# Kernel optimization log

Measured on AMD Instinct MI355X. Metric: run time of the kernel, lower is better.

Reference implementation:

```python
import jax, jax.numpy as jnp
import numpy as np

N = 100000      # nodes
E = 1000000     # edges per relation
D_IN = 128
D_OUT = 128
SLOPE = 0.2
N_REL = 3


def setup_inputs() -> dict:
    key = jax.random.key(0)
    ks = jax.random.split(key, 1 + 4 * N_REL)
    inp = {"H": jax.random.normal(ks[0], (N, D_IN), dtype=jnp.float32)}
    xav_w = float(np.sqrt(6.0 / (D_IN + D_OUT)))   # xavier_uniform bound for W
    xav_a = float(np.sqrt(6.0 / (1 + 2 * D_OUT)))  # xavier_uniform on a viewed as [1, 2d]
    for i in range(N_REL):
        inp[f"row_{i}"] = jax.random.randint(ks[1 + 4 * i], (E,), 0, N, dtype=jnp.int64)
        inp[f"col_{i}"] = jax.random.randint(ks[2 + 4 * i], (E,), 0, N, dtype=jnp.int64)
        inp[f"W_{i}"] = jax.random.uniform(ks[3 + 4 * i], (D_IN, D_OUT), jnp.float32, -xav_w, xav_w)
        inp[f"a_{i}"] = jax.random.uniform(ks[4 + 4 * i], (2 * D_OUT,), jnp.float32, -xav_a, xav_a)
    inp["bias"] = jnp.zeros((D_OUT,), jnp.float32)
    return inp


def _relation_agg(H, W, a, row, col):
    # 1) transform: Wh = H @ W_r  [N, d]
    Wh = H @ W
    d = Wh.shape[1]
    # 2) edge scores: e_ij = leaky_relu(a[:d].Wh[row] + a[d:].Wh[col])
    s_dst = Wh @ a[:d]   # coefficient for destination (row) side  [N]
    s_src = Wh @ a[d:]   # coefficient for source (col) side       [N]
    e = jax.nn.leaky_relu(s_dst[row] + s_src[col], negative_slope=SLOPE)  # [E]
    # 3) segment softmax over incoming edges of each destination node
    e_max = jax.ops.segment_max(e, row, num_segments=N)          # [N]
    e_shift = jnp.exp(e - e_max[row])                            # [E]
    e_sum = jax.ops.segment_sum(e_shift, row, num_segments=N)    # [N]
    alpha = e_shift / jnp.maximum(e_sum[row], 1e-12)             # [E]
    # 4) weighted aggregation of source features
    return jax.ops.segment_sum(alpha[:, None] * Wh[col], row, num_segments=N)  # [N, d]


def reference(H, row_0, col_0, row_1, col_1, row_2, col_2,
              W_0, W_1, W_2, a_0, a_1, a_2, bias):
    rows = (row_0, row_1, row_2)
    cols = (col_0, col_1, col_2)
    Ws = (W_0, W_1, W_2)
    As = (a_0, a_1, a_2)
    agg = jnp.zeros((N, D_OUT), H.dtype)
    for r in range(N_REL):
        agg = agg + _relation_agg(H, Ws[r], As[r], rows[r], cols[r])
    return agg + bias
```

## Files before the change

kernel.cpp:

```cpp
#include <hip/hip_runtime.h>

#define SLOPE 0.2f

typedef unsigned int uint;
typedef unsigned short ushort;
typedef __attribute__((ext_vector_type(8))) short short8;
typedef __attribute__((ext_vector_type(4))) float f32x4;

#define BINW 2048
#define BINSHIFT 11
#define CAP 22528

__device__ inline ushort f2bf(float f) {
    uint u = __float_as_uint(f);
    uint r = (u + 0x7FFFu + ((u >> 16) & 1u)) >> 16;
    return (ushort)r;
}
__device__ inline uint pack2bf(float lo, float hi) {
    return (uint)f2bf(lo) | ((uint)f2bf(hi) << 16);
}
__device__ inline float bfl(uint u) { return __uint_as_float(u << 16); }
__device__ inline float bfh(uint u) { return __uint_as_float(u & 0xFFFF0000u); }

__global__ void wt3(const float* __restrict__ W0, const float* __restrict__ W1,
                    const float* __restrict__ W2,
                    const float* __restrict__ a0, const float* __restrict__ a1,
                    const float* __restrict__ a2,
                    ushort* __restrict__ WT, float* __restrict__ wa,
                    int* __restrict__ bincnt, int nbz) {
    int r = blockIdx.x;
    if (r == 0 && threadIdx.x < nbz) bincnt[threadIdx.x] = 0;
    const float* W = (r == 0) ? W0 : (r == 1) ? W1 : W2;
    const float* a = (r == 0) ? a0 : (r == 1) ? a1 : a2;
    ushort* wt = WT + r * 16384;
    for (int i = threadIdx.x; i < 16384; i += 256) {
        int k = i >> 7, n = i & 127;
        wt[n * 128 + k] = f2bf(W[i]);
    }
    if (threadIdx.x < 128) {
        int k = threadIdx.x;
        const float* wrow = W + k * 128;
        float pd = 0.f, ps = 0.f;
        for (int n = 0; n < 128; n += 4) {
            float4 w4 = *reinterpret_cast<const float4*>(wrow + n);
            float4 aL = *reinterpret_cast<const float4*>(a + n);
            float4 aR = *reinterpret_cast<const float4*>(a + 128 + n);
            pd += w4.x * aL.x + w4.y * aL.y + w4.z * aL.z + w4.w * aL.w;
            ps += w4.x * aR.x + w4.y * aR.y + w4.z * aR.z + w4.w * aR.w;
        }
        wa[r * 256 + k] = pd;
        wa[r * 256 + 128 + k] = ps;
    }
}

__global__ __launch_bounds__(256) void gemm3(const float* __restrict__ H,
                                             const ushort* __restrict__ WT,
                                             ushort* __restrict__ whAll, int N) {
    __shared__ ushort lds[16384];
    const int brow = blockIdx.x * 128;
    const int t = threadIdx.x;

    for (int c = t; c < 2048; c += 256) {
        int r = c >> 4;
        int kb = (c & 15) << 4;
        int gr = brow + r;
        uint4 u = make_uint4(0, 0, 0, 0);
        if (gr < N) {
            const float* hp = H + (size_t)gr * 128 + (kb >> 1);
            float4 v0 = *reinterpret_cast<const float4*>(hp);
            float4 v1 = *reinterpret_cast<const float4*>(hp + 4);
            u.x = pack2bf(v0.x, v0.y);
            u.y = pack2bf(v0.z, v0.w);
            u.z = pack2bf(v1.x, v1.y);
            u.w = pack2bf(v1.z, v1.w);
        }
        int dst = (r << 8) + (kb ^ ((r & 7) << 4));
        *reinterpret_cast<uint4*>((char*)lds + dst) = u;
    }
    __syncthreads();

    const int wave = t >> 6, lane = t & 63;
    const int l16 = lane & 15, lhi = lane >> 4;

    for (int rel = 0; rel < 3; ++rel) {
        ushort* Wh = whAll + (size_t)rel * N * 128;
        const ushort* wt = WT + rel * 16384;

        short8 bf[2][4];
#pragma unroll
        for (int nt = 0; nt < 2; ++nt) {
            int n = wave * 32 + nt * 16 + l16;
#pragma unroll
            for (int ks = 0; ks < 4; ++ks)
                bf[nt][ks] = *reinterpret_cast<const short8*>(wt + n * 128 + ks * 32 + lhi * 8);
        }

        f32x4 acc[8][2];
#pragma unroll
        for (int mt = 0; mt < 8; ++mt) { acc[mt][0] = (f32x4)(0.f); acc[mt][1] = (f32x4)(0.f); }

#pragma unroll
        for (int ks = 0; ks < 4; ++ks) {
#pragma unroll
            for (int mt = 0; mt < 8; ++mt) {
                int r = mt * 16 + l16;
                int kb = (ks * 32 + lhi * 8) * 2;
                int addr = (r << 8) + (kb ^ ((r & 7) << 4));
                short8 af = *reinterpret_cast<const short8*>((char*)lds + addr);
                acc[mt][0] = __builtin_amdgcn_mfma_f32_16x16x32_bf16(af, bf[0][ks], acc[mt][0], 0, 0, 0);
                acc[mt][1] = __builtin_amdgcn_mfma_f32_16x16x32_bf16(af, bf[1][ks], acc[mt][1], 0, 0, 0);
            }
        }

#pragma unroll
        for (int mt = 0; mt < 8; ++mt)
#pragma unroll
            for (int nt = 0; nt < 2; ++nt)
#pragma unroll
                for (int reg = 0; reg < 4; ++reg) {
                    int gr = brow + mt * 16 + lhi * 4 + reg;
                    if (gr < N)
                        Wh[(size_t)gr * 128 + wave * 32 + nt * 16 + l16] = f2bf(acc[mt][nt][reg]);
                }
    }
}

__global__ __launch_bounds__(256) void scores_k(const float* __restrict__ H,
                                                const float* __restrict__ wa,
                                                float* __restrict__ sd,
                                                float* __restrict__ ss, int N) {
    int node = blockIdx.x * 16 + (threadIdx.x >> 4);
    int ql = threadIdx.x & 15;
    if (node >= N) return;
    const float* hp = H + (size_t)node * 128 + ql * 8;
    float4 h0 = *reinterpret_cast<const float4*>(hp);
    float4 h1 = *reinterpret_cast<const float4*>(hp + 4);
#pragma unroll
    for (int r = 0; r < 3; ++r) {
        const float* wd = wa + r * 256 + ql * 8;
        const float* wsv = wa + r * 256 + 128 + ql * 8;
        float4 d0 = *reinterpret_cast<const float4*>(wd);
        float4 d1 = *reinterpret_cast<const float4*>(wd + 4);
        float4 s0 = *reinterpret_cast<const float4*>(wsv);
        float4 s1 = *reinterpret_cast<const float4*>(wsv + 4);
        float pd = h0.x * d0.x + h0.y * d0.y + h0.z * d0.z + h0.w * d0.w +
                   h1.x * d1.x + h1.y * d1.y + h1.z * d1.z + h1.w * d1.w;
        float ps = h0.x * s0.x + h0.y * s0.y + h0.z * s0.z + h0.w * s0.w +
                   h1.x * s1.x + h1.y * s1.y + h1.z * s1.z + h1.w * s1.w;
#pragma unroll
        for (int off = 1; off < 16; off <<= 1) {
            pd += __shfl_xor(pd, off);
            ps += __shfl_xor(ps, off);
        }
        if (ql == 0) { sd[r * N + node] = pd; ss[r * N + node] = ps; }
    }
}

__global__ __launch_bounds__(256) void binscatter(const int* __restrict__ r0, const int* __restrict__ r1,
                                                  const int* __restrict__ r2, const int* __restrict__ c0,
                                                  const int* __restrict__ c1, const int* __restrict__ c2,
                                                  const float* __restrict__ sd, const float* __restrict__ ss,
                                                  int* __restrict__ bincnt, uint2* __restrict__ binned,
                                                  int E, int N, int nbins) {
    __shared__ uint2 staged[4096];
    __shared__ int hist[256], sB[256], curi[256], gbase[256];
    const int t = threadIdx.x;
    hist[t] = 0;
    __syncthreads();

    uint2 rec[16];
    short bn[16];
    const int base = blockIdx.x * 4096;
#pragma unroll
    for (int k = 0; k < 16; ++k) {
        int i = base + k * 256 + t;
        bn[k] = -1;
        if (i < 3 * E) {
            int r = (i >= 2 * E) ? 2 : (i >= E) ? 1 : 0;
            int li = i - r * E;
            const int* rp = (r == 0) ? r0 : (r == 1) ? r1 : r2;
            const int* cp = (r == 0) ? c0 : (r == 1) ? c1 : c2;
            int rr = __builtin_nontemporal_load(rp + li);
            int cc = __builtin_nontemporal_load(cp + li);
            int idx = rr * 3 + r;
            int b = idx >> BINSHIFT;
            uint lo = (uint)(idx & (BINW - 1));
            float x = sd[r * N + rr] + ss[r * N + cc];
            x = (x > 0.f) ? x : SLOPE * x;
            float w = __expf(x);
            rec[k] = make_uint2((uint)cc | (lo << 17), __float_as_uint(w));
            bn[k] = (short)b;
            atomicAdd(&hist[b], 1);
        }
    }
    __syncthreads();

    int v = hist[t];
    int* pa = hist; int* pb = sB;
    for (int off = 1; off < 256; off <<= 1) {
        int x = pa[t] + ((t >= off) ? pa[t - off] : 0);
        pb[t] = x;
        __syncthreads();
        int* tmp = pa; pa = pb; pb = tmp;
    }
    sB[t] = pa[t] - v;
    curi[t] = pa[t] - v;
    if (t < nbins && v > 0) gbase[t] = t * CAP + atomicAdd(&bincnt[t], v);
    __syncthreads();

#pragma unroll
    for (int k = 0; k < 16; ++k)
        if (bn[k] >= 0) {
            int p = atomicAdd(&curi[bn[k]], 1);
            staged[p] = rec[k];
        }
    __syncthreads();

    const int g32 = t >> 5, lane32 = t & 31;
    for (int b = g32; b < nbins; b += 8) {
        int s = sB[b];
        int len = hist[b] - s;
        if (len <= 0) continue;
        int g = gbase[b];
        for (int j = lane32; j < len; j += 32) binned[g + j] = staged[s + j];
    }
}

__global__ __launch_bounds__(256) void binscan(const int* __restrict__ bincnt,
                                               int* __restrict__ binbase, int nbins) {
    __shared__ int sA[256], sB[256];
    int t = threadIdx.x;
    int v = (t < nbins) ? bincnt[t] : 0;
    sA[t] = v;
    __syncthreads();
    int* pa = sA; int* pb = sB;
    for (int off = 1; off < 256; off <<= 1) {
        int x = pa[t] + ((t >= off) ? pa[t - off] : 0);
        pb[t] = x;
        __syncthreads();
        int* tmp = pa; pa = pb; pb = tmp;
    }
    if (t < nbins) binbase[t] = pa[t] - v;
    if (t == nbins - 1) binbase[nbins] = pa[t];
}

__global__ __launch_bounds__(256) void binsort(const uint2* __restrict__ binned,
                                               const int* __restrict__ bincnt,
                                               const int* __restrict__ binbase,
                                               uint2* __restrict__ wc, int* __restrict__ offs,
                                               int L, int N) {
    __shared__ int s1[BINW];
    __shared__ int wsum[4];
    const int b = blockIdx.x, t = threadIdx.x;
    const int cnt = bincnt[b];
    const int dst0 = binbase[b];
    const uint2* src = binned + (size_t)b * CAP;
    const int ibase = b << BINSHIFT;
    const int width = min(BINW, L - ibase);

    for (int i = t; i < BINW; i += 256) s1[i] = 0;
    __syncthreads();
    for (int j = t; j < cnt; j += 256)
        atomicAdd(&s1[(src[j].x >> 17) & (BINW - 1)], 1);
    __syncthreads();

    const int cb = t * 8;
    int v[8];
    int run = 0;
#pragma unroll
    for (int k = 0; k < 8; ++k) { run += s1[cb + k]; v[k] = run; }
    const int lane = t & 63, wv = t >> 6;
    int x = run;
#pragma unroll
    for (int off = 1; off < 64; off <<= 1) {
        int y = __shfl_up(x, off);
        if (lane >= off) x += y;
    }
    if (lane == 63) wsum[wv] = x;
    __syncthreads();
    int pre = x - run;
#pragma unroll
    for (int w = 0; w < 3; ++w) if (wv > w) pre += wsum[w];

#pragma unroll
    for (int k = 0; k < 8; ++k) {
        int i = cb + k;
        if (i < width) offs[ibase + i] = dst0 + pre + v[k];
    }
#pragma unroll
    for (int k = 0; k < 8; ++k)
        s1[cb + k] = dst0 + pre + (k ? v[k - 1] : 0);
    __syncthreads();

    for (int j = t; j < cnt; j += 256) {
        uint2 r = src[j];
        uint lo = (r.x >> 17) & (BINW - 1);
        int p = atomicAdd(&s1[lo], 1);
        int gidx = ibase + (int)lo;
        int rel = gidx - (gidx / 3) * 3;
        uint cc = r.x & 0x1FFFFu;
        wc[p] = make_uint2(r.y, ((uint)(rel * N) + cc) | ((uint)rel << 19));
    }
}

__global__ __launch_bounds__(256) void aggregate3(const uint* __restrict__ whAll,
                                                  const uint2* __restrict__ wc,
                                                  const int* __restrict__ offs,
                                                  const float* __restrict__ bias,
                                                  float* __restrict__ out, int N) {
    int node = blockIdx.x * 16 + (threadIdx.x >> 4);
    int ql = threadIdx.x & 15;
    if (node >= N) return;

    const int base = node * 3;
    const int s0 = (base == 0) ? 0 : offs[base - 1];
    const int s3 = offs[base + 2];

    float w0s = 0.f, w1s = 0.f, w2s = 0.f;
    for (int j = s0; j < s3; ++j) {
        uint2 e = wc[j];
        float w = __uint_as_float(e.x);
        uint rel = e.y >> 19;
        w0s += (rel == 0) ? w : 0.f;
        w1s += (rel == 1) ? w : 0.f;
        w2s += (rel == 2) ? w : 0.f;
    }
    const float inv0 = 1.f / fmaxf(w0s, 1e-12f);
    const float inv1 = 1.f / fmaxf(w1s, 1e-12f);
    const float inv2 = 1.f / fmaxf(w2s, 1e-12f);

    float a0 = 0.f, a1 = 0.f, a2 = 0.f, a3 = 0.f, a4 = 0.f, a5 = 0.f, a6 = 0.f, a7 = 0.f;
    float g0 = 0.f, g1 = 0.f, g2 = 0.f, g3 = 0.f, g4 = 0.f, g5 = 0.f, g6 = 0.f, g7 = 0.f;

    int j = s0;
    for (; j + 4 <= s3; j += 4) {
        uint2 e0 = wc[j], e1 = wc[j + 1], e2 = wc[j + 2], e3 = wc[j + 3];
        uint4 v0 = reinterpret_cast<const uint4*>(whAll + ((size_t)(e0.y & 0x7FFFFu) << 6))[ql];
        uint4 v1 = reinterpret_cast<const uint4*>(whAll + ((size_t)(e1.y & 0x7FFFFu) << 6))[ql];
        uint4 v2 = reinterpret_cast<const uint4*>(whAll + ((size_t)(e2.y & 0x7FFFFu) << 6))[ql];
        uint4 v3 = reinterpret_cast<const uint4*>(whAll + ((size_t)(e3.y & 0x7FFFFu) << 6))[ql];
        uint r0 = e0.y >> 19, r1 = e1.y >> 19, r2 = e2.y >> 19, r3 = e3.y >> 19;
        float w0 = __uint_as_float(e0.x) * ((r0 == 0) ? inv0 : (r0 == 1) ? inv1 : inv2);
        float w1 = __uint_as_float(e1.x) * ((r1 == 0) ? inv0 : (r1 == 1) ? inv1 : inv2);
        float w2 = __uint_as_float(e2.x) * ((r2 == 0) ? inv0 : (r2 == 1) ? inv1 : inv2);
        float w3 = __uint_as_float(e3.x) * ((r3 == 0) ? inv0 : (r3 == 1) ? inv1 : inv2);
        a0 = fmaf(w0, bfl(v0.x), a0); a1 = fmaf(w0, bfh(v0.x), a1);
        a2 = fmaf(w0, bfl(v0.y), a2); a3 = fmaf(w0, bfh(v0.y), a3);
        a4 = fmaf(w0, bfl(v0.z), a4); a5 = fmaf(w0, bfh(v0.z), a5);
        a6 = fmaf(w0, bfl(v0.w), a6); a7 = fmaf(w0, bfh(v0.w), a7);
        g0 = fmaf(w1, bfl(v1.x), g0); g1 = fmaf(w1, bfh(v1.x), g1);
        g2 = fmaf(w1, bfl(v1.y), g2); g3 = fmaf(w1, bfh(v1.y), g3);
        g4 = fmaf(w1, bfl(v1.z), g4); g5 = fmaf(w1, bfh(v1.z), g5);
        g6 = fmaf(w1, bfl(v1.w), g6); g7 = fmaf(w1, bfh(v1.w), g7);
        a0 = fmaf(w2, bfl(v2.x), a0); a1 = fmaf(w2, bfh(v2.x), a1);
        a2 = fmaf(w2, bfl(v2.y), a2); a3 = fmaf(w2, bfh(v2.y), a3);
        a4 = fmaf(w2, bfl(v2.z), a4); a5 = fmaf(w2, bfh(v2.z), a5);
        a6 = fmaf(w2, bfl(v2.w), a6); a7 = fmaf(w2, bfh(v2.w), a7);
        g0 = fmaf(w3, bfl(v3.x), g0); g1 = fmaf(w3, bfh(v3.x), g1);
        g2 = fmaf(w3, bfl(v3.y), g2); g3 = fmaf(w3, bfh(v3.y), g3);
        g4 = fmaf(w3, bfl(v3.z), g4); g5 = fmaf(w3, bfh(v3.z), g5);
        g6 = fmaf(w3, bfl(v3.w), g6); g7 = fmaf(w3, bfh(v3.w), g7);
    }
    for (; j < s3; ++j) {
        uint2 e = wc[j];
        uint r = e.y >> 19;
        float w = __uint_as_float(e.x) * ((r == 0) ? inv0 : (r == 1) ? inv1 : inv2);
        uint4 v = reinterpret_cast<const uint4*>(whAll + ((size_t)(e.y & 0x7FFFFu) << 6))[ql];
        a0 = fmaf(w, bfl(v.x), a0); a1 = fmaf(w, bfh(v.x), a1);
        a2 = fmaf(w, bfl(v.y), a2); a3 = fmaf(w, bfh(v.y), a3);
        a4 = fmaf(w, bfl(v.z), a4); a5 = fmaf(w, bfh(v.z), a5);
        a6 = fmaf(w, bfl(v.w), a6); a7 = fmaf(w, bfh(v.w), a7);
    }

    float4 b0 = *reinterpret_cast<const float4*>(bias + ql * 8);
    float4 b1 = *reinterpret_cast<const float4*>(bias + ql * 8 + 4);
    float* o = out + (size_t)node * 128 + ql * 8;
    f32x4 o0 = {a0 + g0 + b0.x, a1 + g1 + b0.y, a2 + g2 + b0.z, a3 + g3 + b0.w};
    f32x4 o1 = {a4 + g4 + b1.x, a5 + g5 + b1.y, a6 + g6 + b1.z, a7 + g7 + b1.w};
    __builtin_nontemporal_store(o0, reinterpret_cast<f32x4*>(o));
    __builtin_nontemporal_store(o1, reinterpret_cast<f32x4*>(o + 4));
}

extern "C" void kernel_launch(void* const* d_in, const int* in_sizes, int n_in,
                              void* d_out, int out_size, void* d_ws, size_t ws_size,
                              hipStream_t stream) {
    const float* H = (const float*)d_in[0];
    const int* row[3] = {(const int*)d_in[1], (const int*)d_in[5], (const int*)d_in[9]};
    const int* col[3] = {(const int*)d_in[2], (const int*)d_in[6], (const int*)d_in[10]};
    const float* W[3] = {(const float*)d_in[3], (const float*)d_in[7], (const float*)d_in[11]};
    const float* a[3] = {(const float*)d_in[4], (const float*)d_in[8], (const float*)d_in[12]};
    const float* bias = (const float*)d_in[13];

    const int N = in_sizes[0] / 128;
    const int E = in_sizes[1];
    float* out = (float*)d_out;

    const int L = 3 * N;
    const int nbins = (L + BINW - 1) >> BINSHIFT;

    char* ws = (char*)d_ws;
    size_t off = 0;
    auto alloc = [&](size_t bytes) -> void* {
        void* p = ws + off;
        off += (bytes + 255) & ~(size_t)255;
        return p;
    };

    ushort* WT = (ushort*)alloc(3 * 16384 * 2);
    float* wa = (float*)alloc(3 * 256 * 4);
    ushort* whAll = (ushort*)alloc((size_t)3 * N * 128 * 2);
    float* sd = (float*)alloc((size_t)L * 4);
    float* ss = (float*)alloc((size_t)L * 4);
    int* offs = (int*)alloc((size_t)L * 4);
    int* bincnt = (int*)alloc((size_t)(nbins + 2) * 4);
    int* binbase = (int*)alloc((size_t)(nbins + 2) * 4);
    uint2* wc = (uint2*)alloc((size_t)3 * E * 8);
    uint2* binned = (uint2*)d_out;

    const int nbG = (N + 127) / 128;
    const int nbQ = (N + 15) / 16;
    const int nbB = (3 * E + 4095) / 4096;

    wt3<<<3, 256, 0, stream>>>(W[0], W[1], W[2], a[0], a[1], a[2], WT, wa, bincnt, nbins + 2);
    gemm3<<<nbG, 256, 0, stream>>>(H, WT, whAll, N);
    scores_k<<<nbQ, 256, 0, stream>>>(H, wa, sd, ss, N);

    binscatter<<<nbB, 256, 0, stream>>>(row[0], row[1], row[2], col[0], col[1], col[2],
                                        sd, ss, bincnt, binned, E, N, nbins);
    binscan<<<1, 256, 0, stream>>>(bincnt, binbase, nbins);
    binsort<<<nbins, 256, 0, stream>>>(binned, bincnt, binbase, wc, offs, L, N);

    aggregate3<<<nbQ, 256, 0, stream>>>((const uint*)whAll, wc, offs, bias, out, N);
}
```

Measured before the change: 330.8 us.

## Bin edges by relation-major key and fuse softmax normalization into aggregation

Changes the CSR bucketing key from node*3+rel to rel*N+node, so each (relation, destination) segment is contiguous and the relation can be recovered from the bucket range instead of stored bits. The aggregation kernel now walks each relation's segment once, accumulating the softmax denominator alongside the weighted feature sum, and applies the normalization afterwards. This removes the separate first pass over edges that only computed per-relation weight sums. A node's three relation segments are no longer adjacent in memory, and the per-node work now goes through a three-iteration loop with separate bounds loads.

```diff
diff --git a/kernel.cpp b/kernel.cpp
--- a/kernel.cpp
+++ b/kernel.cpp
@@ -182,10 +182,10 @@
             const int* cp = (r == 0) ? c0 : (r == 1) ? c1 : c2;
             int rr = __builtin_nontemporal_load(rp + li);
             int cc = __builtin_nontemporal_load(cp + li);
-            int idx = rr * 3 + r;
+            int idx = r * N + rr;
             int b = idx >> BINSHIFT;
             uint lo = (uint)(idx & (BINW - 1));
-            float x = sd[r * N + rr] + ss[r * N + cc];
+            float x = sd[idx] + ss[r * N + cc];
             x = (x > 0.f) ? x : SLOPE * x;
             float w = __expf(x);
             rec[k] = make_uint2((uint)cc | (lo << 17), __float_as_uint(w));
@@ -297,9 +297,9 @@
         uint lo = (r.x >> 17) & (BINW - 1);
         int p = atomicAdd(&s1[lo], 1);
         int gidx = ibase + (int)lo;
-        int rel = gidx - (gidx / 3) * 3;
+        int rel = (gidx >= 2 * N) ? 2 : (gidx >= N) ? 1 : 0;
         uint cc = r.x & 0x1FFFFu;
-        wc[p] = make_uint2(r.y, ((uint)(rel * N) + cc) | ((uint)rel << 19));
+        wc[p] = make_uint2(r.y, (uint)(rel * N) + cc);
     }
 }
 
@@ -312,71 +312,69 @@
     int ql = threadIdx.x & 15;
     if (node >= N) return;
 
-    const int base = node * 3;
-    const int s0 = (base == 0) ? 0 : offs[base - 1];
-    const int s3 = offs[base + 2];
-
-    float w0s = 0.f, w1s = 0.f, w2s = 0.f;
-    for (int j = s0; j < s3; ++j) {
-        uint2 e = wc[j];
-        float w = __uint_as_float(e.x);
-        uint rel = e.y >> 19;
-        w0s += (rel == 0) ? w : 0.f;
-        w1s += (rel == 1) ? w : 0.f;
-        w2s += (rel == 2) ? w : 0.f;
-    }
-    const float inv0 = 1.f / fmaxf(w0s, 1e-12f);
-    const float inv1 = 1.f / fmaxf(w1s, 1e-12f);
-    const float inv2 = 1.f / fmaxf(w2s, 1e-12f);
-
-    float a0 = 0.f, a1 = 0.f, a2 = 0.f, a3 = 0.f, a4 = 0.f, a5 = 0.f, a6 = 0.f, a7 = 0.f;
-    float g0 = 0.f, g1 = 0.f, g2 = 0.f, g3 = 0.f, g4 = 0.f, g5 = 0.f, g6 = 0.f, g7 = 0.f;
-
-    int j = s0;
-    for (; j + 4 <= s3; j += 4) {
-        uint2 e0 = wc[j], e1 = wc[j + 1], e2 = wc[j + 2], e3 = wc[j + 3];
-        uint4 v0 = reinterpret_cast<const uint4*>(whAll + ((size_t)(e0.y & 0x7FFFFu) << 6))[ql];
-        uint4 v1 = reinterpret_cast<const uint4*>(whAll + ((size_t)(e1.y & 0x7FFFFu) << 6))[ql];
-        uint4 v2 = reinterpret_cast<const uint4*>(whAll + ((size_t)(e2.y & 0x7FFFFu) << 6))[ql];
-        uint4 v3 = reinterpret_cast<const uint4*>(whAll + ((size_t)(e3.y & 0x7FFFFu) << 6))[ql];
-        uint r0 = e0.y >> 19, r1 = e1.y >> 19, r2 = e2.y >> 19, r3 = e3.y >> 19;
-        float w0 = __uint_as_float(e0.x) * ((r0 == 0) ? inv0 : (r0 == 1) ? inv1 : inv2);
-        float w1 = __uint_as_float(e1.x) * ((r1 == 0) ? inv0 : (r1 == 1) ? inv1 : inv2);
-        float w2 = __uint_as_float(e2.x) * ((r2 == 0) ? inv0 : (r2 == 1) ? inv1 : inv2);
-        float w3 = __uint_as_float(e3.x) * ((r3 == 0) ? inv0 : (r3 == 1) ? inv1 : inv2);
-        a0 = fmaf(w0, bfl(v0.x), a0); a1 = fmaf(w0, bfh(v0.x), a1);
-        a2 = fmaf(w0, bfl(v0.y), a2); a3 = fmaf(w0, bfh(v0.y), a3);
-        a4 = fmaf(w0, bfl(v0.z), a4); a5 = fmaf(w0, bfh(v0.z), a5);
-        a6 = fmaf(w0, bfl(v0.w), a6); a7 = fmaf(w0, bfh(v0.w), a7);
-        g0 = fmaf(w1, bfl(v1.x), g0); g1 = fmaf(w1, bfh(v1.x), g1);
-        g2 = fmaf(w1, bfl(v1.y), g2); g3 = fmaf(w1, bfh(v1.y), g3);
-        g4 = fmaf(w1, bfl(v1.z), g4); g5 = fmaf(w1, bfh(v1.z), g5);
-        g6 = fmaf(w1, bfl(v1.w), g6); g7 = fmaf(w1, bfh(v1.w), g7);
-        a0 = fmaf(w2, bfl(v2.x), a0); a1 = fmaf(w2, bfh(v2.x), a1);
-        a2 = fmaf(w2, bfl(v2.y), a2); a3 = fmaf(w2, bfh(v2.y), a3);
-        a4 = fmaf(w2, bfl(v2.z), a4); a5 = fmaf(w2, bfh(v2.z), a5);
-        a6 = fmaf(w2, bfl(v2.w), a6); a7 = fmaf(w2, bfh(v2.w), a7);
-        g0 = fmaf(w3, bfl(v3.x), g0); g1 = fmaf(w3, bfh(v3.x), g1);
-        g2 = fmaf(w3, bfl(v3.y), g2); g3 = fmaf(w3, bfh(v3.y), g3);
-        g4 = fmaf(w3, bfl(v3.z), g4); g5 = fmaf(w3, bfh(v3.z), g5);
-        g6 = fmaf(w3, bfl(v3.w), g6); g7 = fmaf(w3, bfh(v3.w), g7);
-    }
-    for (; j < s3; ++j) {
-        uint2 e = wc[j];
-        uint r = e.y >> 19;
-        float w = __uint_as_float(e.x) * ((r == 0) ? inv0 : (r == 1) ? inv1 : inv2);
-        uint4 v = reinterpret_cast<const uint4*>(whAll + ((size_t)(e.y & 0x7FFFFu) << 6))[ql];
-        a0 = fmaf(w, bfl(v.x), a0); a1 = fmaf(w, bfh(v.x), a1);
-        a2 = fmaf(w, bfl(v.y), a2); a3 = fmaf(w, bfh(v.y), a3);
-        a4 = fmaf(w, bfl(v.z), a4); a5 = fmaf(w, bfh(v.z), a5);
-        a6 = fmaf(w, bfl(v.w), a6); a7 = fmaf(w, bfh(v.w), a7);
+    float t0 = 0.f, t1 = 0.f, t2 = 0.f, t3 = 0.f, t4 = 0.f, t5 = 0.f, t6 = 0.f, t7 = 0.f;
+
+#pragma unroll
+    for (int r = 0; r < 3; ++r) {
+        int idx = r * N + node;
+        int end = offs[idx];
+        int beg = (idx == 0) ? 0 : offs[idx - 1];
+        if (beg >= end) continue;
+
+        float wsA = 0.f, wsB = 0.f;
+        float a0 = 0.f, a1 = 0.f, a2 = 0.f, a3 = 0.f, a4 = 0.f, a5 = 0.f, a6 = 0.f, a7 = 0.f;
+        float g0 = 0.f, g1 = 0.f, g2 = 0.f, g3 = 0.f, g4 = 0.f, g5 = 0.f, g6 = 0.f, g7 = 0.f;
+
+        int j = beg;
+        for (; j + 4 <= end; j += 4) {
+            uint2 e0 = wc[j], e1 = wc[j + 1], e2 = wc[j + 2], e3 = wc[j + 3];
+            uint4 v0 = reinterpret_cast<const uint4*>(whAll + ((size_t)e0.y << 6))[ql];
+            uint4 v1 = reinterpret_cast<const uint4*>(whAll + ((size_t)e1.y << 6))[ql];
+            uint4 v2 = reinterpret_cast<const uint4*>(whAll + ((size_t)e2.y << 6))[ql];
+            uint4 v3 = reinterpret_cast<const uint4*>(whAll + ((size_t)e3.y << 6))[ql];
+            float w0 = __uint_as_float(e0.x), w1 = __uint_as_float(e1.x);
+            float w2 = __uint_as_float(e2.x), w3 = __uint_as_float(e3.x);
+            wsA += w0 + w2;
+            wsB += w1 + w3;
+            a0 = fmaf(w0, bfl(v0.x), a0); a1 = fmaf(w0, bfh(v0.x), a1);
+            a2 = fmaf(w0, bfl(v0.y), a2); a3 = fmaf(w0, bfh(v0.y), a3);
+            a4 = fmaf(w0, bfl(v0.z), a4); a5 = fmaf(w0, bfh(v0.z), a5);
+            a6 = fmaf(w0, bfl(v0.w), a6); a7 = fmaf(w0, bfh(v0.w), a7);
+            g0 = fmaf(w1, bfl(v1.x), g0); g1 = fmaf(w1, bfh(v1.x), g1);
+            g2 = fmaf(w1, bfl(v1.y), g2); g3 = fmaf(w1, bfh(v1.y), g3);
+            g4 = fmaf(w1, bfl(v1.z), g4); g5 = fmaf(w1, bfh(v1.z), g5);
+            g6 = fmaf(w1, bfl(v1.w), g6); g7 = fmaf(w1, bfh(v1.w), g7);
+            a0 = fmaf(w2, bfl(v2.x), a0); a1 = fmaf(w2, bfh(v2.x), a1);
+            a2 = fmaf(w2, bfl(v2.y), a2); a3 = fmaf(w2, bfh(v2.y), a3);
+            a4 = fmaf(w2, bfl(v2.z), a4); a5 = fmaf(w2, bfh(v2.z), a5);
+            a6 = fmaf(w2, bfl(v2.w), a6); a7 = fmaf(w2, bfh(v2.w), a7);
+            g0 = fmaf(w3, bfl(v3.x), g0); g1 = fmaf(w3, bfh(v3.x), g1);
+            g2 = fmaf(w3, bfl(v3.y), g2); g3 = fmaf(w3, bfh(v3.y), g3);
+            g4 = fmaf(w3, bfl(v3.z), g4); g5 = fmaf(w3, bfh(v3.z), g5);
+            g6 = fmaf(w3, bfl(v3.w), g6); g7 = fmaf(w3, bfh(v3.w), g7);
+        }
+        for (; j < end; ++j) {
+            uint2 e = wc[j];
+            float w = __uint_as_float(e.x);
+            uint4 v = reinterpret_cast<const uint4*>(whAll + ((size_t)e.y << 6))[ql];
+            wsA += w;
+            a0 = fmaf(w, bfl(v.x), a0); a1 = fmaf(w, bfh(v.x), a1);
+            a2 = fmaf(w, bfl(v.y), a2); a3 = fmaf(w, bfh(v.y), a3);
+            a4 = fmaf(w, bfl(v.z), a4); a5 = fmaf(w, bfh(v.z), a5);
+            a6 = fmaf(w, bfl(v.w), a6); a7 = fmaf(w, bfh(v.w), a7);
+        }
+        float inv = 1.f / fmaxf(wsA + wsB, 1e-12f);
+        t0 = fmaf(a0 + g0, inv, t0); t1 = fmaf(a1 + g1, inv, t1);
+        t2 = fmaf(a2 + g2, inv, t2); t3 = fmaf(a3 + g3, inv, t3);
+        t4 = fmaf(a4 + g4, inv, t4); t5 = fmaf(a5 + g5, inv, t5);
+        t6 = fmaf(a6 + g6, inv, t6); t7 = fmaf(a7 + g7, inv, t7);
     }
 
     float4 b0 = *reinterpret_cast<const float4*>(bias + ql * 8);
     float4 b1 = *reinterpret_cast<const float4*>(bias + ql * 8 + 4);
     float* o = out + (size_t)node * 128 + ql * 8;
-    f32x4 o0 = {a0 + g0 + b0.x, a1 + g1 + b0.y, a2 + g2 + b0.z, a3 + g3 + b0.w};
-    f32x4 o1 = {a4 + g4 + b1.x, a5 + g5 + b1.y, a6 + g6 + b1.z, a7 + g7 + b1.w};
+    f32x4 o0 = {t0 + b0.x, t1 + b0.y, t2 + b0.z, t3 + b0.w};
+    f32x4 o1 = {t4 + b1.x, t5 + b1.y, t6 + b1.z, t7 + b1.w};
     __builtin_nontemporal_store(o0, reinterpret_cast<f32x4*>(o));
     __builtin_nontemporal_store(o1, reinterpret_cast<f32x4*>(o + 4));
 }
```

Result: faster. 283.7 us (median of 2 runs) (-14.3%).
